# Kernel tuning notes

Hardware: AMD Instinct MI355X
Metric: run time of the kernel (lower is better)

The kernel has to match this reference:

```python
import jax, jax.numpy as jnp
import numpy as np

INPUT_SIZE, HIDDEN_SIZE, OUTPUT_SIZE, K = 64, 128, 64, 3


def causal_conv1d(x_bcs, w, b, k):
    # x_bcs: (B, C, S); w: (H, C*k) in torch Linear layout (flat index = c*k + j)
    B, C, S = x_bcs.shape
    xp = jnp.pad(x_bcs, ((0, 0), (0, 0), (k - 1, 0)))  # causal left pad
    # windows: (B, C, k, S) -- window j holds xp[:, :, j:j+S]
    windows = jnp.stack([xp[:, :, j:j + S] for j in range(k)], axis=2)
    wk = w.reshape(w.shape[0], C, k)  # (H, C, k), matches view(B, -1) flattening
    return jnp.einsum('bcks,hck->bhs', windows, wk) + b[None, :, None]


def setup_inputs() -> dict:
    key = jax.random.key(0)
    ks = jax.random.split(key, 7)
    def lin(kw, kb, fan_in, fan_out):
        bound = 1.0 / np.sqrt(fan_in)
        w = jax.random.uniform(kw, (fan_out, fan_in), jnp.float32, -bound, bound)
        b = jax.random.uniform(kb, (fan_out,), jnp.float32, -bound, bound)
        return w, b
    x = jax.random.normal(ks[0], (16, 16384, INPUT_SIZE), jnp.float32)
    conv1_w, conv1_b = lin(ks[1], ks[2], INPUT_SIZE * K, HIDDEN_SIZE)
    conv2_w, conv2_b = lin(ks[3], ks[4], HIDDEN_SIZE * K, HIDDEN_SIZE)
    fc_w, fc_b = lin(ks[5], ks[6], HIDDEN_SIZE, OUTPUT_SIZE)
    return {"x": x, "conv1_w": conv1_w, "conv1_b": conv1_b,
            "conv2_w": conv2_w, "conv2_b": conv2_b,
            "fc_w": fc_w, "fc_b": fc_b}


def reference(x, conv1_w, conv1_b, conv2_w, conv2_b, fc_w, fc_b):
    h = x.transpose(0, 2, 1)                         # (B, C_in, S)
    h = jax.nn.relu(causal_conv1d(h, conv1_w, conv1_b, K))
    h = jax.nn.relu(causal_conv1d(h, conv2_w, conv2_b, K))
    last = h[:, :, -1]                               # (B, H)
    return last @ fc_w.T + fc_b                      # (B, output_size)
```

## Files before the change

kernel.cpp:

```cpp
#include <hip/hip_runtime.h>
#include <hip/hip_bf16.h>


#define S_LEN   16384
#define C_IN    64
#define HID     128
#define C_OUT   64
#define KW      3

__global__ __launch_bounds__(512)
void tcn_tail_kernel(const float* __restrict__ x,
                     const float* __restrict__ w1, const float* __restrict__ b1,
                     const float* __restrict__ w2, const float* __restrict__ b2,
                     const float* __restrict__ fw, const float* __restrict__ fb,
                     float* __restrict__ out)
{
    const int b   = blockIdx.x;
    const int tid = threadIdx.x;

    __shared__ float xf[3][C_IN * KW];
    __shared__ float h1f[HID * KW];
    __shared__ float h2s[HID];

    const float* xb = x + (size_t)b * S_LEN * C_IN + (size_t)(S_LEN - 5) * C_IN;
    if (tid < 5 * C_IN) {
        const float v = xb[tid];
        const int s = tid >> 6;
        const int c = tid & 63;
        #pragma unroll
        for (int t = 0; t < 3; ++t) {
            const int j = s - t;
            if (0 <= j && j < KW) xf[t][c * KW + j] = v;
        }
    }
    __syncthreads();

    {
        const int h = tid >> 2;
        const int q = tid & 3;
        const float4* wv = (const float4*)(w1 + (size_t)h * (C_IN * KW));
        float a0 = 0.f, a1 = 0.f, a2 = 0.f;
        #pragma unroll
        for (int m = 0; m < 12; ++m) {
            const int ch = m * 4 + q;
            const float4 w  = wv[ch];
            const float4 p0 = ((const float4*)xf[0])[ch];
            const float4 p1 = ((const float4*)xf[1])[ch];
            const float4 p2 = ((const float4*)xf[2])[ch];
            a0 += w.x * p0.x + w.y * p0.y + w.z * p0.z + w.w * p0.w;
            a1 += w.x * p1.x + w.y * p1.y + w.z * p1.z + w.w * p1.w;
            a2 += w.x * p2.x + w.y * p2.y + w.z * p2.z + w.w * p2.w;
        }
        a0 += __shfl_xor(a0, 1); a0 += __shfl_xor(a0, 2);
        a1 += __shfl_xor(a1, 1); a1 += __shfl_xor(a1, 2);
        a2 += __shfl_xor(a2, 1); a2 += __shfl_xor(a2, 2);
        if (q == 0) {
            const float bb = b1[h];
            h1f[h * KW + 0] = fmaxf(a0 + bb, 0.f);
            h1f[h * KW + 1] = fmaxf(a1 + bb, 0.f);
            h1f[h * KW + 2] = fmaxf(a2 + bb, 0.f);
        }
    }
    __syncthreads();

    {
        const int h = tid >> 2;
        const int q = tid & 3;
        const float4* wv = (const float4*)(w2 + (size_t)h * (HID * KW));
        const float4* hv = (const float4*)h1f;
        float a0 = 0.f, a1 = 0.f, a2 = 0.f, a3 = 0.f;
        #pragma unroll
        for (int m = 0; m < 24; m += 4) {
            const int c0 = (m + 0) * 4 + q;
            const int c1 = (m + 1) * 4 + q;
            const int c2 = (m + 2) * 4 + q;
            const int c3 = (m + 3) * 4 + q;
            const float4 w0 = wv[c0], w1v = wv[c1], w2v = wv[c2], w3v = wv[c3];
            const float4 p0 = hv[c0], p1 = hv[c1], p2 = hv[c2], p3 = hv[c3];
            a0 += w0.x * p0.x + w0.y * p0.y + w0.z * p0.z + w0.w * p0.w;
            a1 += w1v.x * p1.x + w1v.y * p1.y + w1v.z * p1.z + w1v.w * p1.w;
            a2 += w2v.x * p2.x + w2v.y * p2.y + w2v.z * p2.z + w2v.w * p2.w;
            a3 += w3v.x * p3.x + w3v.y * p3.y + w3v.z * p3.z + w3v.w * p3.w;
        }
        float a = (a0 + a1) + (a2 + a3);
        a += __shfl_xor(a, 1); a += __shfl_xor(a, 2);
        if (q == 0) h2s[h] = fmaxf(a + b2[h], 0.f);
    }
    __syncthreads();

    {
        const int o = tid >> 3;
        const int r = tid & 7;
        const float4* wv = (const float4*)(fw + (size_t)o * HID);
        const float4* hv = (const float4*)h2s;
        float a = 0.f;
        #pragma unroll
        for (int m = 0; m < 4; ++m) {
            const int ch = m * 8 + r;
            const float4 w  = wv[ch];
            const float4 p  = hv[ch];
            a += w.x * p.x + w.y * p.y + w.z * p.z + w.w * p.w;
        }
        a += __shfl_xor(a, 1); a += __shfl_xor(a, 2); a += __shfl_xor(a, 4);
        if (r == 0) out[(size_t)b * C_OUT + o] = a + fb[o];
    }
}

extern "C" void kernel_launch(void* const* d_in, const int* in_sizes, int n_in,
                              void* d_out, int out_size, void* d_ws, size_t ws_size,
                              hipStream_t stream) {
    const float* x  = (const float*)d_in[0];
    const float* w1 = (const float*)d_in[1];
    const float* b1 = (const float*)d_in[2];
    const float* w2 = (const float*)d_in[3];
    const float* b2 = (const float*)d_in[4];
    const float* fw = (const float*)d_in[5];
    const float* fb = (const float*)d_in[6];
    float* out = (float*)d_out;

    tcn_tail_kernel<<<16, 512, 0, stream>>>(x, w1, b1, w2, b2, fw, fb, out);
}
```

Baseline: 9.342 us.

## Prefetch conv2 and fc weights into registers before input load, use 1024 threads

Weights for the second conv and the final linear layer are now loaded into registers at kernel start. Their global-memory latency can then overlap the input gather and the first conv instead of stalling on the critical path after each barrier. The block grows to 1024 threads, with 8 threads per hidden unit and 16 per output, which halves the per-thread dot-product length but adds one more shuffle-reduction stage. Register pressure rises because 14 float4 values are held per thread at 1024-thread occupancy.

Result: slower. 9.849 us (+5.4%).

```diff
diff --git a/kernel.cpp b/kernel.cpp
--- a/kernel.cpp
+++ b/kernel.cpp
@@ -8,7 +8,7 @@
 #define C_OUT   64
 #define KW      3
 
-__global__ __launch_bounds__(512)
+__global__ __launch_bounds__(1024)
 void tcn_tail_kernel(const float* __restrict__ x,
                      const float* __restrict__ w1, const float* __restrict__ b1,
                      const float* __restrict__ w2, const float* __restrict__ b2,
@@ -21,6 +21,26 @@
     __shared__ float xf[3][C_IN * KW];
     __shared__ float h1f[HID * KW];
     __shared__ float h2s[HID];
+
+    const int h8 = tid >> 3;
+    const int q8 = tid & 7;
+    const int o16 = tid >> 4;
+    const int r16 = tid & 15;
+
+    float4 pw[12];
+    {
+        const float4* wv = (const float4*)(w2 + (size_t)h8 * (HID * KW));
+        #pragma unroll
+        for (int m = 0; m < 12; ++m)
+            pw[m] = wv[m * 8 + q8];
+    }
+    float4 pf[2];
+    {
+        const float4* wv = (const float4*)(fw + (size_t)o16 * HID);
+        #pragma unroll
+        for (int m = 0; m < 2; ++m)
+            pf[m] = wv[m * 16 + r16];
+    }
 
     const float* xb = x + (size_t)b * S_LEN * C_IN + (size_t)(S_LEN - 5) * C_IN;
     if (tid < 5 * C_IN) {
@@ -36,13 +56,11 @@
     __syncthreads();
 
     {
-        const int h = tid >> 2;
-        const int q = tid & 3;
-        const float4* wv = (const float4*)(w1 + (size_t)h * (C_IN * KW));
+        const float4* wv = (const float4*)(w1 + (size_t)h8 * (C_IN * KW));
         float a0 = 0.f, a1 = 0.f, a2 = 0.f;
         #pragma unroll
-        for (int m = 0; m < 12; ++m) {
-            const int ch = m * 4 + q;
+        for (int m = 0; m < 6; ++m) {
+            const int ch = m * 8 + q8;
             const float4 w  = wv[ch];
             const float4 p0 = ((const float4*)xf[0])[ch];
             const float4 p1 = ((const float4*)xf[1])[ch];
@@ -51,58 +69,49 @@
             a1 += w.x * p1.x + w.y * p1.y + w.z * p1.z + w.w * p1.w;
             a2 += w.x * p2.x + w.y * p2.y + w.z * p2.z + w.w * p2.w;
         }
-        a0 += __shfl_xor(a0, 1); a0 += __shfl_xor(a0, 2);
-        a1 += __shfl_xor(a1, 1); a1 += __shfl_xor(a1, 2);
-        a2 += __shfl_xor(a2, 1); a2 += __shfl_xor(a2, 2);
-        if (q == 0) {
-            const float bb = b1[h];
-            h1f[h * KW + 0] = fmaxf(a0 + bb, 0.f);
-            h1f[h * KW + 1] = fmaxf(a1 + bb, 0.f);
-            h1f[h * KW + 2] = fmaxf(a2 + bb, 0.f);
+        a0 += __shfl_xor(a0, 1); a0 += __shfl_xor(a0, 2); a0 += __shfl_xor(a0, 4);
+        a1 += __shfl_xor(a1, 1); a1 += __shfl_xor(a1, 2); a1 += __shfl_xor(a1, 4);
+        a2 += __shfl_xor(a2, 1); a2 += __shfl_xor(a2, 2); a2 += __shfl_xor(a2, 4);
+        if (q8 == 0) {
+            const float bb = b1[h8];
+            h1f[h8 * KW + 0] = fmaxf(a0 + bb, 0.f);
+            h1f[h8 * KW + 1] = fmaxf(a1 + bb, 0.f);
+            h1f[h8 * KW + 2] = fmaxf(a2 + bb, 0.f);
         }
     }
     __syncthreads();
 
     {
-        const int h = tid >> 2;
-        const int q = tid & 3;
-        const float4* wv = (const float4*)(w2 + (size_t)h * (HID * KW));
         const float4* hv = (const float4*)h1f;
         float a0 = 0.f, a1 = 0.f, a2 = 0.f, a3 = 0.f;
         #pragma unroll
-        for (int m = 0; m < 24; m += 4) {
-            const int c0 = (m + 0) * 4 + q;
-            const int c1 = (m + 1) * 4 + q;
-            const int c2 = (m + 2) * 4 + q;
-            const int c3 = (m + 3) * 4 + q;
-            const float4 w0 = wv[c0], w1v = wv[c1], w2v = wv[c2], w3v = wv[c3];
-            const float4 p0 = hv[c0], p1 = hv[c1], p2 = hv[c2], p3 = hv[c3];
+        for (int m = 0; m < 12; m += 4) {
+            const float4 p0 = hv[(m + 0) * 8 + q8];
+            const float4 p1 = hv[(m + 1) * 8 + q8];
+            const float4 p2 = hv[(m + 2) * 8 + q8];
+            const float4 p3 = hv[(m + 3) * 8 + q8];
+            const float4 w0 = pw[m + 0], w1v = pw[m + 1];
+            const float4 w2v = pw[m + 2], w3v = pw[m + 3];
             a0 += w0.x * p0.x + w0.y * p0.y + w0.z * p0.z + w0.w * p0.w;
             a1 += w1v.x * p1.x + w1v.y * p1.y + w1v.z * p1.z + w1v.w * p1.w;
             a2 += w2v.x * p2.x + w2v.y * p2.y + w2v.z * p2.z + w2v.w * p2.w;
             a3 += w3v.x * p3.x + w3v.y * p3.y + w3v.z * p3.z + w3v.w * p3.w;
         }
         float a = (a0 + a1) + (a2 + a3);
-        a += __shfl_xor(a, 1); a += __shfl_xor(a, 2);
-        if (q == 0) h2s[h] = fmaxf(a + b2[h], 0.f);
+        a += __shfl_xor(a, 1); a += __shfl_xor(a, 2); a += __shfl_xor(a, 4);
+        if (q8 == 0) h2s[h8] = fmaxf(a + b2[h8], 0.f);
     }
     __syncthreads();
 
     {
-        const int o = tid >> 3;
-        const int r = tid & 7;
-        const float4* wv = (const float4*)(fw + (size_t)o * HID);
         const float4* hv = (const float4*)h2s;
-        float a = 0.f;
-        #pragma unroll
-        for (int m = 0; m < 4; ++m) {
-            const int ch = m * 8 + r;
-            const float4 w  = wv[ch];
-            const float4 p  = hv[ch];
-            a += w.x * p.x + w.y * p.y + w.z * p.z + w.w * p.w;
-        }
-        a += __shfl_xor(a, 1); a += __shfl_xor(a, 2); a += __shfl_xor(a, 4);
-        if (r == 0) out[(size_t)b * C_OUT + o] = a + fb[o];
+        const float4 p0 = hv[0 * 16 + r16];
+        const float4 p1 = hv[1 * 16 + r16];
+        float a = pf[0].x * p0.x + pf[0].y * p0.y + pf[0].z * p0.z + pf[0].w * p0.w
+                + pf[1].x * p1.x + pf[1].y * p1.y + pf[1].z * p1.z + pf[1].w * p1.w;
+        a += __shfl_xor(a, 1); a += __shfl_xor(a, 2);
+        a += __shfl_xor(a, 4); a += __shfl_xor(a, 8);
+        if (r16 == 0) out[(size_t)b * C_OUT + o16] = a + fb[o16];
     }
 }
 
@@ -118,5 +127,5 @@
     const float* fb = (const float*)d_in[6];
     float* out = (float*)d_out;
 
-    tcn_tail_kernel<<<16, 512, 0, stream>>>(x, w1, b1, w2, b2, fw, fb, out);
+    tcn_tail_kernel<<<16, 1024, 0, stream>>>(x, w1, b1, w2, b2, fw, fb, out);
 }
```
